# Performance work log

Hardware: AMD Instinct MI355X
Metric: run time of the kernel (lower is better)

Reference implementation:

```python
import jax, jax.numpy as jnp
import numpy as np

B, CIN, H, W = 32, 128, 64, 64
OUT, KH, KW = 256, 3, 3
NSK, SDIM = 4, 128


def setup_inputs() -> dict:
    key = jax.random.key(0)
    kx, kw_, kb, ks = jax.random.split(key, 4)
    x = jax.random.normal(kx, (B, CIN, H, W), dtype=jnp.float32)
    kval = float(np.sqrt(1.0 / (CIN * KH * KW)))  # groups=1
    weight = jax.random.uniform(kw_, (OUT, CIN, KH, KW), jnp.float32, -kval, kval)
    bias_tensor = jax.random.uniform(kb, (OUT,), jnp.float32, -kval, kval)
    # Rademacher / sketch_dim, shape (n, s, O) == torch's type1_signed_matrices
    signed = (2.0 * jax.random.bernoulli(ks, 0.5, (NSK, SDIM, OUT)).astype(jnp.float32) - 1.0) / SDIM
    # prod = einsum('ijkl,mi->mjkl') per sketch -> (n, s, Cin, kh, kw)
    prod = jnp.einsum('oikl,nso->nsikl', weight, signed)
    # .permute(2,3,1,0).flatten(0,2): (s,Cin,kh,kw) -> (kh,kw,Cin,s) -> (kh*kw*Cin, s)
    type1_sketches = prod.transpose(0, 3, 4, 2, 1).reshape(NSK, KH * KW * CIN, SDIM)
    return {
        "x": x,
        "type1_sketches": type1_sketches,
        "type1_signed_matrices": signed,
        "bias_tensor": bias_tensor,
    }


def reference(x, type1_sketches, type1_signed_matrices, bias_tensor):
    b, _, h1, w1 = x.shape
    h2 = h1 - KH + 1
    w2 = w1 - KW + 1
    # torch unfold: (B, Cin*KH*KW, E), features ordered channel-major (C, kh, kw)
    patches = jax.lax.conv_general_dilated_patches(
        x, filter_shape=(KH, KW), window_strides=(1, 1), padding='VALID'
    )  # (B, Cin*KH*KW, H2, W2)
    patches = patches.reshape(b, CIN * KH * KW, h2 * w2)  # (B, F, E)
    # 'bnfe,nfs->bnse' with the n-expansion folded away
    y = jnp.einsum('bfe,nfs->bnse', patches, type1_sketches)
    z = jnp.einsum('bnse,nso->bnoe', y, type1_signed_matrices)
    z = z.reshape(b, NSK, OUT, h2, w2)
    out = jnp.mean(z, axis=1) + bias_tensor[None, :, None, None]
    return out
```

## Files before the change

### kernel.cpp

```cpp
#include <hip/hip_runtime.h>
#include <hip/hip_bf16.h>
#include <stdint.h>


#define BATCH 32
#define CIN   128
#define HH    64
#define WW    64
#define OUTC  256
#define H2    62
#define W2    62
#define A_TILE 16384
#define WS_A_BYTES (36 * A_TILE)
#define BROWB 16384

typedef __bf16 bf16x8 __attribute__((ext_vector_type(8)));
typedef float  f32x4  __attribute__((ext_vector_type(4)));

typedef unsigned int u32_as1 __attribute__((address_space(1)));
typedef unsigned int u32_as3 __attribute__((address_space(3)));

__device__ __forceinline__ void async_copy16(const void* g, void* l) {
  __builtin_amdgcn_global_load_lds((const u32_as1*)g, (u32_as3*)l, 16, 0, 0);
}

#define FPB 4
__global__ __launch_bounds__(256) void weff_kernel(
    const float* __restrict__ sketches,
    const float* __restrict__ sgn,
    char* __restrict__ wsA)
{
  __shared__ alignas(16) float sk[512 * FPB];
  const int f0 = blockIdx.x * FPB;
  const int t  = threadIdx.x;

  for (int k = 0; k < (512 * FPB) / 256; ++k) {
    int idx = t + k * 256;
    int fi  = idx >> 9;
    int ns  = idx & 511;
    int n   = ns >> 7;
    int s   = ns & 127;
    sk[ns * FPB + fi] = sketches[(n * 1152 + f0 + fi) * 128 + s];
  }
  __syncthreads();

  const int o = t;
  float acc0 = 0.f, acc1 = 0.f, acc2 = 0.f, acc3 = 0.f;
#pragma unroll 8
  for (int ns = 0; ns < 512; ++ns) {
    float sg = sgn[ns * 256 + o];
    f32x4 skv = *(const f32x4*)(&sk[ns * FPB]);
    acc0 += sg * skv[0];
    acc1 += sg * skv[1];
    acc2 += sg * skv[2];
    acc3 += sg * skv[3];
  }

  float accs[FPB] = {acc0, acc1, acc2, acc3};
#pragma unroll
  for (int fi = 0; fi < FPB; ++fi) {
    int f   = f0 + fi;
    int c   = f / 9;
    int tap = f - c * 9;
    int st  = tap * 4 + (c >> 5);
    int kk  = c & 31;
    uint32_t byteoff = (uint32_t)st * A_TILE + (uint32_t)(o >> 4) * 1024
                     + (uint32_t)(((kk >> 3) * 16 + (o & 15)) * 16)
                     + (uint32_t)((kk & 7) * 2);
    *(__hip_bfloat16*)(wsA + byteoff) = __float2bfloat16(accs[fi] * 0.25f);
  }
}

__global__ __launch_bounds__(256, 2) void conv_kernel(
    const float* __restrict__ x,
    const char*  __restrict__ wA,
    const float* __restrict__ bias,
    float* __restrict__ out)
{
  __shared__ alignas(16) char lds[2 * A_TILE + 3 * BROWB];
  char* ldsA = lds;
  char* ldsB = lds + 2 * A_TILE;

  const int bid = blockIdx.x;
  const int swz = (bid & 7) * 248 + (bid >> 3);
  const int b   = swz / H2;
  const int i   = swz - b * H2;

  const int t    = threadIdx.x;
  const int lane = t & 63;
  const int w    = t >> 6;

#define STAGE_A(ST, BUF) do {                                              \
    const char* asrc_ = wA + (size_t)(ST) * A_TILE + w * 4096 + lane * 16; \
    char* adst_ = ldsA + (BUF) * A_TILE + w * 4096;                        \
    async_copy16(asrc_,         adst_);                                    \
    async_copy16(asrc_ + 1024,  adst_ + 1024);                             \
    async_copy16(asrc_ + 2048,  adst_ + 2048);                             \
    async_copy16(asrc_ + 3072,  adst_ + 3072);                             \
  } while (0)

  STAGE_A(0, 0);

  {
    const int j  = t & 63;
    const int cq = t >> 6;
    const uint32_t swb = (uint32_t)((j & 7) << 4);
#pragma unroll
    for (int r = 0; r < 3; ++r) {
      const float* xr = x + (((size_t)(b * CIN + cq * 32)) * HH + (i + r)) * WW + j;
      char* lrow = ldsB + r * BROWB + j * 256;
#pragma unroll
      for (int g = 0; g < 4; ++g) {
        bf16x8 pk;
#pragma unroll
        for (int cc = 0; cc < 8; ++cc)
          pk[cc] = (__bf16)xr[(size_t)(g * 8 + cc) * (HH * WW)];
        uint32_t c0b = (uint32_t)(cq * 64 + g * 16);
        *(bf16x8*)(lrow + (c0b ^ swb)) = pk;
      }
    }
  }

  f32x4 acc[4][4];
  const f32x4 zf = {0.f, 0.f, 0.f, 0.f};
#pragma unroll
  for (int mi = 0; mi < 4; ++mi)
#pragma unroll
    for (int ni = 0; ni < 4; ++ni)
      acc[mi][ni] = zf;

  const int ln15  = lane & 15;
  const int khi16 = (lane >> 4) << 4;
  const char* pA = ldsA + w * 4096 + lane * 16;

#define MKB(COL, PAR) (ldsB + (COL) * 256                                  \
    + (uint32_t)((((PAR) * 64) | khi16) ^ (((COL) & 7) << 4)))
  const char* pB00 = MKB(ln15 + 0, 0); const char* pB01 = MKB(ln15 + 0, 1);
  const char* pB10 = MKB(ln15 + 1, 0); const char* pB11 = MKB(ln15 + 1, 1);
  const char* pB20 = MKB(ln15 + 2, 0); const char* pB21 = MKB(ln15 + 2, 1);
  const int c30 = (48 + ln15 + 0 > 63) ? 63 : 48 + ln15 + 0;
  const int c31 = (48 + ln15 + 1 > 63) ? 63 : 48 + ln15 + 1;
  const int c32 = (48 + ln15 + 2 > 63) ? 63 : 48 + ln15 + 2;
  const char* pC00 = MKB(c30, 0); const char* pC01 = MKB(c30, 1);
  const char* pC10 = MKB(c31, 0); const char* pC11 = MKB(c31, 1);
  const char* pC20 = MKB(c32, 0); const char* pC21 = MKB(c32, 1);
#undef MKB

  __syncthreads();

#define MFMA_ __builtin_amdgcn_mfma_f32_16x16x32_bf16

#define STEP(ST, KH, KW, CK2, PAR) do {                                    \
    if ((ST) < 35) STAGE_A((ST) + 1, ((ST) + 1) & 1);                      \
    const int ab_ = ((ST) & 1) * A_TILE;                                   \
    const int bi_ = (KH) * BROWB + (CK2) * 128;                            \
    bf16x8 b0_ = *(const bf16x8*)(pB##KW##PAR + bi_);                      \
    bf16x8 b1_ = *(const bf16x8*)(pB##KW##PAR + bi_ + 4096);               \
    bf16x8 b2_ = *(const bf16x8*)(pB##KW##PAR + bi_ + 8192);               \
    bf16x8 b3_ = *(const bf16x8*)(pC##KW##PAR + bi_);                      \
    bf16x8 a0_ = *(const bf16x8*)(pA + ab_);                               \
    bf16x8 a1_ = *(const bf16x8*)(pA + ab_ + 1024);                        \
    bf16x8 a2_ = *(const bf16x8*)(pA + ab_ + 2048);                        \
    bf16x8 a3_ = *(const bf16x8*)(pA + ab_ + 3072);                        \
    __builtin_amdgcn_s_setprio(1);                                         \
    acc[0][0] = MFMA_(a0_, b0_, acc[0][0], 0, 0, 0);                       \
    acc[0][1] = MFMA_(a0_, b1_, acc[0][1], 0, 0, 0);                       \
    acc[0][2] = MFMA_(a0_, b2_, acc[0][2], 0, 0, 0);                       \
    acc[0][3] = MFMA_(a0_, b3_, acc[0][3], 0, 0, 0);                       \
    acc[1][0] = MFMA_(a1_, b0_, acc[1][0], 0, 0, 0);                       \
    acc[1][1] = MFMA_(a1_, b1_, acc[1][1], 0, 0, 0);                       \
    acc[1][2] = MFMA_(a1_, b2_, acc[1][2], 0, 0, 0);                       \
    acc[1][3] = MFMA_(a1_, b3_, acc[1][3], 0, 0, 0);                       \
    acc[2][0] = MFMA_(a2_, b0_, acc[2][0], 0, 0, 0);                       \
    acc[2][1] = MFMA_(a2_, b1_, acc[2][1], 0, 0, 0);                       \
    acc[2][2] = MFMA_(a2_, b2_, acc[2][2], 0, 0, 0);                       \
    acc[2][3] = MFMA_(a2_, b3_, acc[2][3], 0, 0, 0);                       \
    acc[3][0] = MFMA_(a3_, b0_, acc[3][0], 0, 0, 0);                       \
    acc[3][1] = MFMA_(a3_, b1_, acc[3][1], 0, 0, 0);                       \
    acc[3][2] = MFMA_(a3_, b2_, acc[3][2], 0, 0, 0);                       \
    acc[3][3] = MFMA_(a3_, b3_, acc[3][3], 0, 0, 0);                       \
    __builtin_amdgcn_s_setprio(0);                                         \
    if ((ST) < 35) __syncthreads();                                        \
  } while (0)

  STEP(0,  0, 0, 0, 0);  STEP(1,  0, 0, 0, 1);
  STEP(2,  0, 0, 1, 0);  STEP(3,  0, 0, 1, 1);
  STEP(4,  0, 1, 0, 0);  STEP(5,  0, 1, 0, 1);
  STEP(6,  0, 1, 1, 0);  STEP(7,  0, 1, 1, 1);
  STEP(8,  0, 2, 0, 0);  STEP(9,  0, 2, 0, 1);
  STEP(10, 0, 2, 1, 0);  STEP(11, 0, 2, 1, 1);
  STEP(12, 1, 0, 0, 0);  STEP(13, 1, 0, 0, 1);
  STEP(14, 1, 0, 1, 0);  STEP(15, 1, 0, 1, 1);
  STEP(16, 1, 1, 0, 0);  STEP(17, 1, 1, 0, 1);
  STEP(18, 1, 1, 1, 0);  STEP(19, 1, 1, 1, 1);
  STEP(20, 1, 2, 0, 0);  STEP(21, 1, 2, 0, 1);
  STEP(22, 1, 2, 1, 0);  STEP(23, 1, 2, 1, 1);
  STEP(24, 2, 0, 0, 0);  STEP(25, 2, 0, 0, 1);
  STEP(26, 2, 0, 1, 0);  STEP(27, 2, 0, 1, 1);
  STEP(28, 2, 1, 0, 0);  STEP(29, 2, 1, 0, 1);
  STEP(30, 2, 1, 1, 0);  STEP(31, 2, 1, 1, 1);
  STEP(32, 2, 2, 0, 0);  STEP(33, 2, 2, 0, 1);
  STEP(34, 2, 2, 1, 0);  STEP(35, 2, 2, 1, 1);

#undef STEP
#undef MFMA_
#undef STAGE_A

  const int jn = ln15;
  const int g4 = lane >> 4;
#pragma unroll
  for (int mi = 0; mi < 4; ++mi) {
#pragma unroll
    for (int ni = 0; ni < 4; ++ni) {
      const int jj = (ni << 4) + jn;
      if (jj < W2) {
#pragma unroll
        for (int rr = 0; rr < 4; ++rr) {
          const int o = (w << 6) + (mi << 4) + (g4 << 2) + rr;
          out[(((size_t)b * OUTC + o) * H2 + i) * W2 + jj] =
              acc[mi][ni][rr] + bias[o];
        }
      }
    }
  }
}

extern "C" void kernel_launch(void* const* d_in, const int* in_sizes, int n_in,
                              void* d_out, int out_size, void* d_ws, size_t ws_size,
                              hipStream_t stream) {
  const float* x        = (const float*)d_in[0];
  const float* sketches = (const float*)d_in[1];
  const float* sgn      = (const float*)d_in[2];
  const float* bias     = (const float*)d_in[3];
  float* out            = (float*)d_out;
  char* wsA             = (char*)d_ws;

  if (ws_size < (size_t)WS_A_BYTES) return;

  weff_kernel<<<1152 / FPB, 256, 0, stream>>>(sketches, sgn, wsA);
  conv_kernel<<<BATCH * H2, 256, 0, stream>>>(x, wsA, bias, out);
}
```

Before: 124.7 us.

## Compute four output rows per block with 8 waves and 4-stage weight pipeline

Each conv block now has 512 threads and covers four output rows instead of one. It stages six input rows in LDS, and each weight tile staged in LDS is reused across the four rows, so weight traffic per output drops. The weight stream moves to a 4-buffer async pipeline with explicit vmcnt/lgkmcnt waits and split barriers, and fragments are register double-buffered so loads overlap the MFMAs. In exchange it uses much more LDS (about 160 KB), 8x4 accumulator tiles per wave raise register pressure, and the last row group does redundant clamped work.

```diff
diff --git a/kernel.cpp b/kernel.cpp
--- a/kernel.cpp
+++ b/kernel.cpp
@@ -13,6 +13,7 @@
 #define A_TILE 16384
 #define WS_A_BYTES (36 * A_TILE)
 #define BROWB 16384
+#define AMAX  (35 * A_TILE)
 
 typedef __bf16 bf16x8 __attribute__((ext_vector_type(8)));
 typedef float  f32x4  __attribute__((ext_vector_type(4)));
@@ -71,70 +72,76 @@
   }
 }
 
-__global__ __launch_bounds__(256, 2) void conv_kernel(
+__global__ __launch_bounds__(512, 2) void conv_kernel(
     const float* __restrict__ x,
     const char*  __restrict__ wA,
     const float* __restrict__ bias,
     float* __restrict__ out)
 {
-  __shared__ alignas(16) char lds[2 * A_TILE + 3 * BROWB];
+  __shared__ alignas(16) char lds[4 * A_TILE + 6 * BROWB];
   char* ldsA = lds;
-  char* ldsB = lds + 2 * A_TILE;
+  char* ldsB = lds + 4 * A_TILE;
 
   const int bid = blockIdx.x;
-  const int swz = (bid & 7) * 248 + (bid >> 3);
-  const int b   = swz / H2;
-  const int i   = swz - b * H2;
+  const int swz = (bid & 7) * 64 + (bid >> 3);
+  const int b   = swz >> 4;
+  const int ig  = swz & 15;
+  const int i0  = ig * 4;
 
   const int t    = threadIdx.x;
   const int lane = t & 63;
   const int w    = t >> 6;
-
-#define STAGE_A(ST, BUF) do {                                              \
-    const char* asrc_ = wA + (size_t)(ST) * A_TILE + w * 4096 + lane * 16; \
-    char* adst_ = ldsA + (BUF) * A_TILE + w * 4096;                        \
-    async_copy16(asrc_,         adst_);                                    \
-    async_copy16(asrc_ + 1024,  adst_ + 1024);                             \
-    async_copy16(asrc_ + 2048,  adst_ + 2048);                             \
-    async_copy16(asrc_ + 3072,  adst_ + 3072);                             \
+  const int wm   = w >> 2;
+  const int we   = w & 3;
+
+  const char* aSrcLane = wA + w * 2048 + lane * 16;
+
+#define STAGE(AOFF, TGT) do {                                              \
+    const char* s_ = aSrcLane + (AOFF);                                    \
+    char* d_ = ldsA + (TGT) * A_TILE + w * 2048;                           \
+    async_copy16(s_,        d_);                                           \
+    async_copy16(s_ + 1024, d_ + 1024);                                    \
   } while (0)
 
-  STAGE_A(0, 0);
+  STAGE(0, 0);
+  STAGE(A_TILE, 1);
+  STAGE(2 * A_TILE, 2);
 
   {
     const int j  = t & 63;
     const int cq = t >> 6;
     const uint32_t swb = (uint32_t)((j & 7) << 4);
 #pragma unroll
-    for (int r = 0; r < 3; ++r) {
-      const float* xr = x + (((size_t)(b * CIN + cq * 32)) * HH + (i + r)) * WW + j;
+    for (int r = 0; r < 6; ++r) {
+      int xrow = i0 + r; if (xrow > 63) xrow = 63;
+      const float* xr = x + (((size_t)(b * CIN + cq * 16)) * HH + xrow) * WW + j;
       char* lrow = ldsB + r * BROWB + j * 256;
 #pragma unroll
-      for (int g = 0; g < 4; ++g) {
+      for (int g = 0; g < 2; ++g) {
         bf16x8 pk;
 #pragma unroll
         for (int cc = 0; cc < 8; ++cc)
           pk[cc] = (__bf16)xr[(size_t)(g * 8 + cc) * (HH * WW)];
-        uint32_t c0b = (uint32_t)(cq * 64 + g * 16);
+        uint32_t c0b = (uint32_t)(cq * 32 + g * 16);
         *(bf16x8*)(lrow + (c0b ^ swb)) = pk;
       }
     }
   }
 
-  f32x4 acc[4][4];
+  f32x4 acc[8][4];
   const f32x4 zf = {0.f, 0.f, 0.f, 0.f};
 #pragma unroll
-  for (int mi = 0; mi < 4; ++mi)
+  for (int mi = 0; mi < 8; ++mi)
 #pragma unroll
     for (int ni = 0; ni < 4; ++ni)
       acc[mi][ni] = zf;
 
   const int ln15  = lane & 15;
   const int khi16 = (lane >> 4) << 4;
-  const char* pA = ldsA + w * 4096 + lane * 16;
-
-#define MKB(COL, PAR) (ldsB + (COL) * 256                                  \
-    + (uint32_t)((((PAR) * 64) | khi16) ^ (((COL) & 7) << 4)))
+  const char* pA = ldsA + wm * 8192 + lane * 16;
+
+#define MKB(COL, PAR) (ldsB + we * BROWB + (COL) * 256                     \
+    + (uint32_t)(((((PAR) * 64) | khi16) ^ (((COL) & 7) << 4))))
   const char* pB00 = MKB(ln15 + 0, 0); const char* pB01 = MKB(ln15 + 0, 1);
   const char* pB10 = MKB(ln15 + 1, 0); const char* pB11 = MKB(ln15 + 1, 1);
   const char* pB20 = MKB(ln15 + 2, 0); const char* pB21 = MKB(ln15 + 2, 1);
@@ -148,77 +155,134 @@
 
   __syncthreads();
 
+  bf16x8 aX0, aX1, aX2, aX3, aY0, aY1, aY2, aY3, b0, b1, b2, b3;
+
+  aX0 = *(const bf16x8*)(pA);
+  aX1 = *(const bf16x8*)(pA + 1024);
+  aX2 = *(const bf16x8*)(pA + 2048);
+  aX3 = *(const bf16x8*)(pA + 3072);
+  b0  = *(const bf16x8*)(pB00);
+  b1  = *(const bf16x8*)(pB00 + 4096);
+  b2  = *(const bf16x8*)(pB00 + 8192);
+  b3  = *(const bf16x8*)(pC00);
+
+  uint32_t aoff = 3 * A_TILE;
+
 #define MFMA_ __builtin_amdgcn_mfma_f32_16x16x32_bf16
-
-#define STEP(ST, KH, KW, CK2, PAR) do {                                    \
-    if ((ST) < 35) STAGE_A((ST) + 1, ((ST) + 1) & 1);                      \
-    const int ab_ = ((ST) & 1) * A_TILE;                                   \
-    const int bi_ = (KH) * BROWB + (CK2) * 128;                            \
-    bf16x8 b0_ = *(const bf16x8*)(pB##KW##PAR + bi_);                      \
-    bf16x8 b1_ = *(const bf16x8*)(pB##KW##PAR + bi_ + 4096);               \
-    bf16x8 b2_ = *(const bf16x8*)(pB##KW##PAR + bi_ + 8192);               \
-    bf16x8 b3_ = *(const bf16x8*)(pC##KW##PAR + bi_);                      \
-    bf16x8 a0_ = *(const bf16x8*)(pA + ab_);                               \
-    bf16x8 a1_ = *(const bf16x8*)(pA + ab_ + 1024);                        \
-    bf16x8 a2_ = *(const bf16x8*)(pA + ab_ + 2048);                        \
-    bf16x8 a3_ = *(const bf16x8*)(pA + ab_ + 3072);                        \
+#define LGKM0 asm volatile("s_waitcnt lgkmcnt(0)" ::: "memory")
+#define VM2   asm volatile("s_waitcnt vmcnt(2)" ::: "memory")
+
+#define MFMA16(A0_, A1_, A2_, A3_, M_) do {                                \
     __builtin_amdgcn_s_setprio(1);                                         \
-    acc[0][0] = MFMA_(a0_, b0_, acc[0][0], 0, 0, 0);                       \
-    acc[0][1] = MFMA_(a0_, b1_, acc[0][1], 0, 0, 0);                       \
-    acc[0][2] = MFMA_(a0_, b2_, acc[0][2], 0, 0, 0);                       \
-    acc[0][3] = MFMA_(a0_, b3_, acc[0][3], 0, 0, 0);                       \
-    acc[1][0] = MFMA_(a1_, b0_, acc[1][0], 0, 0, 0);                       \
-    acc[1][1] = MFMA_(a1_, b1_, acc[1][1], 0, 0, 0);                       \
-    acc[1][2] = MFMA_(a1_, b2_, acc[1][2], 0, 0, 0);                       \
-    acc[1][3] = MFMA_(a1_, b3_, acc[1][3], 0, 0, 0);                       \
-    acc[2][0] = MFMA_(a2_, b0_, acc[2][0], 0, 0, 0);                       \
-    acc[2][1] = MFMA_(a2_, b1_, acc[2][1], 0, 0, 0);                       \
-    acc[2][2] = MFMA_(a2_, b2_, acc[2][2], 0, 0, 0);                       \
-    acc[2][3] = MFMA_(a2_, b3_, acc[2][3], 0, 0, 0);                       \
-    acc[3][0] = MFMA_(a3_, b0_, acc[3][0], 0, 0, 0);                       \
-    acc[3][1] = MFMA_(a3_, b1_, acc[3][1], 0, 0, 0);                       \
-    acc[3][2] = MFMA_(a3_, b2_, acc[3][2], 0, 0, 0);                       \
-    acc[3][3] = MFMA_(a3_, b3_, acc[3][3], 0, 0, 0);                       \
+    acc[(M_)+0][0] = MFMA_(A0_, b0, acc[(M_)+0][0], 0, 0, 0);              \
+    acc[(M_)+0][1] = MFMA_(A0_, b1, acc[(M_)+0][1], 0, 0, 0);              \
+    acc[(M_)+0][2] = MFMA_(A0_, b2, acc[(M_)+0][2], 0, 0, 0);              \
+    acc[(M_)+0][3] = MFMA_(A0_, b3, acc[(M_)+0][3], 0, 0, 0);              \
+    acc[(M_)+1][0] = MFMA_(A1_, b0, acc[(M_)+1][0], 0, 0, 0);              \
+    acc[(M_)+1][1] = MFMA_(A1_, b1, acc[(M_)+1][1], 0, 0, 0);              \
+    acc[(M_)+1][2] = MFMA_(A1_, b2, acc[(M_)+1][2], 0, 0, 0);              \
+    acc[(M_)+1][3] = MFMA_(A1_, b3, acc[(M_)+1][3], 0, 0, 0);              \
+    acc[(M_)+2][0] = MFMA_(A2_, b0, acc[(M_)+2][0], 0, 0, 0);              \
+    acc[(M_)+2][1] = MFMA_(A2_, b1, acc[(M_)+2][1], 0, 0, 0);              \
+    acc[(M_)+2][2] = MFMA_(A2_, b2, acc[(M_)+2][2], 0, 0, 0);              \
+    acc[(M_)+2][3] = MFMA_(A2_, b3, acc[(M_)+2][3], 0, 0, 0);              \
+    acc[(M_)+3][0] = MFMA_(A3_, b0, acc[(M_)+3][0], 0, 0, 0);              \
+    acc[(M_)+3][1] = MFMA_(A3_, b1, acc[(M_)+3][1], 0, 0, 0);              \
+    acc[(M_)+3][2] = MFMA_(A3_, b2, acc[(M_)+3][2], 0, 0, 0);              \
+    acc[(M_)+3][3] = MFMA_(A3_, b3, acc[(M_)+3][3], 0, 0, 0);              \
     __builtin_amdgcn_s_setprio(0);                                         \
-    if ((ST) < 35) __syncthreads();                                        \
   } while (0)
 
-  STEP(0,  0, 0, 0, 0);  STEP(1,  0, 0, 0, 1);
-  STEP(2,  0, 0, 1, 0);  STEP(3,  0, 0, 1, 1);
-  STEP(4,  0, 1, 0, 0);  STEP(5,  0, 1, 0, 1);
-  STEP(6,  0, 1, 1, 0);  STEP(7,  0, 1, 1, 1);
-  STEP(8,  0, 2, 0, 0);  STEP(9,  0, 2, 0, 1);
-  STEP(10, 0, 2, 1, 0);  STEP(11, 0, 2, 1, 1);
-  STEP(12, 1, 0, 0, 0);  STEP(13, 1, 0, 0, 1);
-  STEP(14, 1, 0, 1, 0);  STEP(15, 1, 0, 1, 1);
-  STEP(16, 1, 1, 0, 0);  STEP(17, 1, 1, 0, 1);
-  STEP(18, 1, 1, 1, 0);  STEP(19, 1, 1, 1, 1);
-  STEP(20, 1, 2, 0, 0);  STEP(21, 1, 2, 0, 1);
-  STEP(22, 1, 2, 1, 0);  STEP(23, 1, 2, 1, 1);
-  STEP(24, 2, 0, 0, 0);  STEP(25, 2, 0, 0, 1);
-  STEP(26, 2, 0, 1, 0);  STEP(27, 2, 0, 1, 1);
-  STEP(28, 2, 1, 0, 0);  STEP(29, 2, 1, 0, 1);
-  STEP(30, 2, 1, 1, 0);  STEP(31, 2, 1, 1, 1);
-  STEP(32, 2, 2, 0, 0);  STEP(33, 2, 2, 0, 1);
-  STEP(34, 2, 2, 1, 0);  STEP(35, 2, 2, 1, 1);
-
-#undef STEP
+#define STEPQ(Q, KWN, PARN, CK2N) do {                                     \
+    VM2;                                                                   \
+    __builtin_amdgcn_s_barrier();                                          \
+    STAGE(aoff, (Q + 3) & 3);                                              \
+    aoff += A_TILE; if (aoff > AMAX) aoff = AMAX;                          \
+    LGKM0;                                                                 \
+    MFMA16(aX0, aX1, aX2, aX3, 0);                                         \
+    aY0 = *(const bf16x8*)(pA + (Q & 3) * A_TILE + 4096);                  \
+    aY1 = *(const bf16x8*)(pA + (Q & 3) * A_TILE + 5120);                  \
+    aY2 = *(const bf16x8*)(pA + (Q & 3) * A_TILE + 6144);                  \
+    aY3 = *(const bf16x8*)(pA + (Q & 3) * A_TILE + 7168);                  \
+    __builtin_amdgcn_s_barrier();                                          \
+    LGKM0;                                                                 \
+    MFMA16(aY0, aY1, aY2, aY3, 4);                                         \
+    aX0 = *(const bf16x8*)(pA + ((Q + 1) & 3) * A_TILE);                   \
+    aX1 = *(const bf16x8*)(pA + ((Q + 1) & 3) * A_TILE + 1024);            \
+    aX2 = *(const bf16x8*)(pA + ((Q + 1) & 3) * A_TILE + 2048);            \
+    aX3 = *(const bf16x8*)(pA + ((Q + 1) & 3) * A_TILE + 3072);            \
+    b0 = *(const bf16x8*)(pB##KWN##PARN + (CK2N) * 128);                   \
+    b1 = *(const bf16x8*)(pB##KWN##PARN + (CK2N) * 128 + 4096);            \
+    b2 = *(const bf16x8*)(pB##KWN##PARN + (CK2N) * 128 + 8192);            \
+    b3 = *(const bf16x8*)(pC##KWN##PARN + (CK2N) * 128);                   \
+  } while (0)
+
+#pragma unroll 1
+  for (int kh = 0; kh < 3; ++kh) {
+    STEPQ(0, 0, 1, 0);
+    STEPQ(1, 0, 0, 1);
+    STEPQ(2, 0, 1, 1);
+    STEPQ(3, 1, 0, 0);
+    STEPQ(4, 1, 1, 0);
+    STEPQ(5, 1, 0, 1);
+    STEPQ(6, 1, 1, 1);
+    STEPQ(7, 2, 0, 0);
+    STEPQ(8, 2, 1, 0);
+    STEPQ(9, 2, 0, 1);
+    STEPQ(10, 2, 1, 1);
+    {
+      VM2;
+      __builtin_amdgcn_s_barrier();
+      STAGE(aoff, (11 + 3) & 3);
+      aoff += A_TILE; if (aoff > AMAX) aoff = AMAX;
+      LGKM0;
+      MFMA16(aX0, aX1, aX2, aX3, 0);
+      aY0 = *(const bf16x8*)(pA + (11 & 3) * A_TILE + 4096);
+      aY1 = *(const bf16x8*)(pA + (11 & 3) * A_TILE + 5120);
+      aY2 = *(const bf16x8*)(pA + (11 & 3) * A_TILE + 6144);
+      aY3 = *(const bf16x8*)(pA + (11 & 3) * A_TILE + 7168);
+      __builtin_amdgcn_s_barrier();
+      LGKM0;
+      MFMA16(aY0, aY1, aY2, aY3, 4);
+      if (kh < 2) {
+        pB00 += BROWB; pB01 += BROWB; pB10 += BROWB; pB11 += BROWB;
+        pB20 += BROWB; pB21 += BROWB; pC00 += BROWB; pC01 += BROWB;
+        pC10 += BROWB; pC11 += BROWB; pC20 += BROWB; pC21 += BROWB;
+      }
+      aX0 = *(const bf16x8*)(pA);
+      aX1 = *(const bf16x8*)(pA + 1024);
+      aX2 = *(const bf16x8*)(pA + 2048);
+      aX3 = *(const bf16x8*)(pA + 3072);
+      b0 = *(const bf16x8*)(pB00);
+      b1 = *(const bf16x8*)(pB00 + 4096);
+      b2 = *(const bf16x8*)(pB00 + 8192);
+      b3 = *(const bf16x8*)(pC00);
+    }
+  }
+
+#undef STEPQ
+#undef MFMA16
+#undef VM2
+#undef LGKM0
 #undef MFMA_
-#undef STAGE_A
-
-  const int jn = ln15;
-  const int g4 = lane >> 4;
-#pragma unroll
-  for (int mi = 0; mi < 4; ++mi) {
-#pragma unroll
-    for (int ni = 0; ni < 4; ++ni) {
-      const int jj = (ni << 4) + jn;
-      if (jj < W2) {
-#pragma unroll
-        for (int rr = 0; rr < 4; ++rr) {
-          const int o = (w << 6) + (mi << 4) + (g4 << 2) + rr;
-          out[(((size_t)b * OUTC + o) * H2 + i) * W2 + jj] =
-              acc[mi][ni][rr] + bias[o];
+#undef STAGE
+
+  const int jn   = ln15;
+  const int g4   = lane >> 4;
+  const int irow = i0 + we;
+  if (irow < H2) {
+#pragma unroll
+    for (int mi = 0; mi < 8; ++mi) {
+#pragma unroll
+      for (int ni = 0; ni < 4; ++ni) {
+        const int jj = (ni << 4) + jn;
+        if (jj < W2) {
+#pragma unroll
+          for (int rr = 0; rr < 4; ++rr) {
+            const int o = (wm << 7) + (mi << 4) + (g4 << 2) + rr;
+            out[(((size_t)b * OUTC + o) * H2 + irow) * W2 + jj] =
+                acc[mi][ni][rr] + bias[o];
+          }
         }
       }
     }
@@ -238,5 +302,5 @@
   if (ws_size < (size_t)WS_A_BYTES) return;
 
   weff_kernel<<<1152 / FPB, 256, 0, stream>>>(sketches, sgn, wsA);
-  conv_kernel<<<BATCH * H2, 256, 0, stream>>>(x, wsA, bias, out);
+  conv_kernel<<<BATCH * 16, 512, 0, stream>>>(x, wsA, bias, out);
 }
```

Result: faster. 105.3 us (-15.5%).
